# Kernel tuning notes

Measured on AMD Instinct MI355X. Metric: run time of the kernel, lower is better.

Reference implementation:

```python
import jax, jax.numpy as jnp
import numpy as np

EPS = 1e-12  # torch F.normalize eps

def _l2norm(t):
    # normalize over last axis (N), clamp norm like torch.nn.functional.normalize
    n = jnp.linalg.norm(t, axis=-1, keepdims=True)
    return t / jnp.maximum(n, EPS)

def setup_inputs() -> dict:
    key = jax.random.key(0)
    ks = jax.random.split(key, 4)
    B, N, D, H = 8, 4096, 768, 16
    x = jax.random.normal(ks[0], (B, N, D), dtype=jnp.float32)
    w_qkv = jax.random.normal(ks[1], (D, 3 * D), dtype=jnp.float32) * (D ** -0.5)
    temperature = jnp.ones((H, 1, 1), dtype=jnp.float32)
    w_proj = jax.random.normal(ks[2], (D, D), dtype=jnp.float32) * (D ** -0.5)
    b_proj = jnp.zeros((D,), dtype=jnp.float32)
    return {"x": x, "w_qkv": w_qkv, "temperature": temperature,
            "w_proj": w_proj, "b_proj": b_proj}

def reference(x, w_qkv, temperature, w_proj, b_proj):
    B, N, D = x.shape
    H = temperature.shape[0]
    C = D // H
    # qkv linear (no bias), split last dim as (3, H, C), move to (3, B, H, C, N)
    qkv = (x @ w_qkv).reshape(B, N, 3, H, C).transpose(2, 0, 3, 4, 1)
    q, k, v = qkv[0], qkv[1], qkv[2]            # each [B, H, C, N]
    q = _l2norm(q)
    k = _l2norm(k)
    # cross-covariance attention: small CxC matrix per head
    attn = jnp.einsum('bhcn,bhdn->bhcd', q, k) * temperature  # [B,H,C,C]
    attn = jax.nn.softmax(attn, axis=-1)
    out = jnp.einsum('bhcd,bhdn->bhcn', attn, v)  # [B,H,C,N]
    out = out.transpose(0, 3, 1, 2).reshape(B, N, D)  # B N (H C)
    return out @ w_proj + b_proj
```

## Files before the change

kernel.cpp:

```cpp
#include <hip/hip_runtime.h>
#include <stdint.h>

typedef __attribute__((ext_vector_type(4))) float          f32x4;
typedef __attribute__((ext_vector_type(8))) short          bf16x8;
typedef __attribute__((ext_vector_type(8))) unsigned short u16x8;
typedef __attribute__((ext_vector_type(4))) unsigned short u16x4;
typedef __attribute__((ext_vector_type(2))) long           longx2;

static __device__ __forceinline__ unsigned short f2bf(float f){
  uint32_t u = __builtin_bit_cast(uint32_t, f);
  u += 0x7FFFu + ((u >> 16) & 1u);
  return (unsigned short)(u >> 16);
}
static __device__ __forceinline__ float bf2f(unsigned short h){
  uint32_t u = ((uint32_t)h) << 16;
  return __builtin_bit_cast(float, u);
}

static __device__ __forceinline__ uint32_t f2e4m3(float x){
  uint32_t u = __builtin_bit_cast(uint32_t, x);
  uint32_t s = (u >> 24) & 0x80u;
  uint32_t a = u & 0x7FFFFFFFu;
  if (a >= 0x43E00000u) return s | 0x7Eu;
  int ebits = (int)(a >> 23);
  uint32_t mfull = (a & 0x7FFFFFu) | 0x800000u;
  int shift = (ebits >= 121) ? 20 : 20 + (121 - ebits);
  if (shift > 31) return s;
  uint32_t q = mfull >> shift;
  uint32_t rem = mfull & ((1u << shift) - 1u);
  uint32_t half = 1u << (shift - 1);
  q += (rem > half || (rem == half && (q & 1u)));
  if (ebits >= 121){
    uint32_t E = (uint32_t)(ebits - 121 + 1);
    if (q == 16u){ E += 1u; q = 8u; }
    uint32_t man = q - 8u;
    if (E > 15u || (E == 15u && man == 7u)) return s | 0x7Eu;
    return s | (E << 3) | man;
  } else {
    if (q >= 8u) return s | (1u << 3) | (q - 8u);
    return s | q;
  }
}
static __device__ __forceinline__ uint32_t pk4_e4m3(float a0, float a1, float a2, float a3){
#if __has_builtin(__builtin_amdgcn_cvt_pk_fp8_f32)
  uint32_t pk = (uint32_t)__builtin_amdgcn_cvt_pk_fp8_f32(a0, a1, 0, false);
  pk = (uint32_t)__builtin_amdgcn_cvt_pk_fp8_f32(a2, a3, (int)pk, true);
  return pk;
#else
  return f2e4m3(a0) | (f2e4m3(a1) << 8) | (f2e4m3(a2) << 16) | (f2e4m3(a3) << 24);
#endif
}

#define GLL(SRC, DST) __builtin_amdgcn_global_load_lds(                         \
    (const __attribute__((address_space(1))) unsigned int*)(SRC),               \
    (__attribute__((address_space(3))) unsigned int*)(DST), 16, 0, 0)

__global__ void k_pre(const float* __restrict__ x, const float* __restrict__ wqkv,
                      const float* __restrict__ wproj,
                      unsigned short* __restrict__ xbf, unsigned char* __restrict__ x8,
                      unsigned char* __restrict__ WT8, unsigned short* __restrict__ WpT,
                      unsigned short* __restrict__ WvB)
{
  __shared__ float tl[64][65];
  const int bx = blockIdx.x, t = threadIdx.x;
  if (bx < 12288){
    const long i = ((long)bx * 256 + t) * 8;
    const f32x4* p = (const f32x4*)(x + i);
    f32x4 a = p[0], b = p[1];
    u16x8 o;
    #pragma unroll
    for (int j = 0; j < 4; j++){ o[j] = f2bf(a[j]); o[4+j] = f2bf(b[j]); }
    *(u16x8*)(xbf + i) = o;
    uint32_t p0 = pk4_e4m3(a[0], a[1], a[2], a[3]);
    uint32_t p1 = pk4_e4m3(b[0], b[1], b[2], b[3]);
    *(uint32_t*)(x8 + i)     = p0;
    *(uint32_t*)(x8 + i + 4) = p1;
  } else if (bx < 12720){
    const int idx = bx - 12288;
    const int cb = idx % 36, rb = idx / 36;
    const int qk = (cb < 24);
    const float* in = qk ? wqkv : wproj;
    const int C = qk ? 2304 : 768;
    const int c0 = (qk ? cb : cb - 24) * 64, r0 = rb * 64;
    {
      const int lr = t >> 2, lc = (t & 3) * 16;
      const f32x4* s = (const f32x4*)(in + (long)(r0 + lr) * C + c0 + lc);
      #pragma unroll
      for (int q = 0; q < 4; q++){
        f32x4 v = s[q];
        #pragma unroll
        for (int j = 0; j < 4; j++) tl[lr][lc + q*4 + j] = v[j];
      }
    }
    __syncthreads();
    {
      const int oc = t >> 2, orr = (t & 3) * 16;
      if (qk){
        uint32_t w0 = pk4_e4m3(tl[orr+0][oc],  tl[orr+1][oc],  tl[orr+2][oc],  tl[orr+3][oc]);
        uint32_t w1 = pk4_e4m3(tl[orr+4][oc],  tl[orr+5][oc],  tl[orr+6][oc],  tl[orr+7][oc]);
        uint32_t w2 = pk4_e4m3(tl[orr+8][oc],  tl[orr+9][oc],  tl[orr+10][oc], tl[orr+11][oc]);
        uint32_t w3 = pk4_e4m3(tl[orr+12][oc], tl[orr+13][oc], tl[orr+14][oc], tl[orr+15][oc]);
        uint32_t* d = (uint32_t*)(WT8 + (long)(c0 + oc) * 768 + r0 + orr);
        d[0] = w0; d[1] = w1; d[2] = w2; d[3] = w3;
      } else {
        u16x8 o0, o1;
        #pragma unroll
        for (int i = 0; i < 8; i++){ o0[i] = f2bf(tl[orr + i][oc]); o1[i] = f2bf(tl[orr + 8 + i][oc]); }
        u16x8* dst = (u16x8*)(WpT + (long)(c0 + oc) * 768 + r0 + orr);
        dst[0] = o0; dst[1] = o1;
      }
    }
  } else {
    const long idx = ((long)(bx - 12720) * 256 + t) * 8;
    const int e = (int)(idx / 768), hd = (int)(idx - (long)e * 768);
    const float* s = wqkv + (long)e * 2304 + 1536 + hd;
    f32x4 a = *(const f32x4*)s, b = *(const f32x4*)(s + 4);
    u16x8 o;
    #pragma unroll
    for (int j = 0; j < 4; j++){ o[j] = f2bf(a[j]); o[4+j] = f2bf(b[j]); }
    *(u16x8*)(WvB + idx) = o;
  }
}

static __device__ __forceinline__ bf16x8 ldfrag(const char* slot, int row, int ko){
  const int k2 = (ko ^ (row >> 1)) & 3;
  return *(const bf16x8*)(slot + row*64 + k2*16);
}
static __device__ __forceinline__ longx2 ldfrag8(const char* slot, int row, int ko){
  const int k2 = (ko ^ (row >> 1)) & 3;
  return *(const longx2*)(slot + row*64 + k2*16);
}

static __device__ __forceinline__ void stg8(const unsigned char* __restrict__ G, int row0, int keB,
                                            char* lds_slot, int t){
  #pragma unroll
  for (int l = 0; l < 2; l++){
    const int r = l*128 + (t >> 2);
    const int c = (t & 3) ^ ((r >> 1) & 3);
    GLL((const char*)(G + (long)(row0 + r) * 768 + keB + c * 16),
        lds_slot + l*8192 + (t & 0x1C0) * 16);
  }
}

#define PH8(BUF, KK, MH, STAGE_STMT, WAIT_STMT) do {                           \
    longx2 af[4];                                                              \
    if (MH == 0) {                                                             \
      _Pragma("unroll")                                                        \
      for (int ni = 0; ni < 4; ni++)                                           \
        bq[ni] = ldfrag8(sB[BUF][KK], wn*64 + ni*16 + arow, ko);               \
    }                                                                          \
    _Pragma("unroll")                                                          \
    for (int mi = 0; mi < 4; mi++)                                             \
      af[mi] = ldfrag8(sA[BUF][KK], wm*128 + MH*64 + mi*16 + arow, ko);        \
    __builtin_amdgcn_s_barrier();                                              \
    __builtin_amdgcn_s_setprio(1);                                             \
    _Pragma("unroll")                                                          \
    for (int mi = 0; mi < 4; mi++)                                             \
      _Pragma("unroll")                                                        \
      for (int ni = 0; ni < 4; ni++){                                          \
        acc[MH*4+mi][ni] = __builtin_amdgcn_mfma_f32_16x16x32_fp8_fp8(         \
            af[mi][0], bq[ni][0], acc[MH*4+mi][ni], 0, 0, 0);                  \
        acc[MH*4+mi][ni] = __builtin_amdgcn_mfma_f32_16x16x32_fp8_fp8(         \
            af[mi][1], bq[ni][1], acc[MH*4+mi][ni], 0, 0, 0);                  \
      }                                                                        \
    __builtin_amdgcn_s_setprio(0);                                             \
    STAGE_STMT;                                                                \
    WAIT_STMT;                                                                 \
    __builtin_amdgcn_s_barrier();                                              \
  } while(0)

__global__ __launch_bounds__(512, 2)
void k_gemm256(const unsigned char* __restrict__ A8, const unsigned char* __restrict__ BT8,
               unsigned char* __restrict__ QT8, unsigned char* __restrict__ KT8,
               float* __restrict__ nrmp)
{
  __shared__ __attribute__((aligned(16))) char lds[131072];
  const int o  = blockIdx.x;
  const int wg = (o & 7) * 96 + (o >> 3);
  const int jt = wg % 6, mt = wg / 6;
  const int m0 = mt * 256, j0 = jt * 256;
  const int t = threadIdx.x, lane = t & 63, w = t >> 6;
  const int wm = w >> 2, wn = w & 3;
  const int arow = lane & 15, ko = lane >> 4;

  char* const sA[2][2] = {{lds,           lds + 16384},
                          {lds + 65536,   lds + 65536 + 16384}};
  char* const sB[2][2] = {{lds + 32768,   lds + 49152},
                          {lds + 65536 + 32768, lds + 65536 + 49152}};

  f32x4 acc[8][4] = {};

  stg8(BT8, j0, 0,   sB[0][0], t);
  stg8(A8,  m0, 0,   sA[0][0], t);
  stg8(BT8, j0, 64,  sB[0][1], t);
  stg8(A8,  m0, 64,  sA[0][1], t);
  stg8(BT8, j0, 128, sB[1][0], t);
  stg8(A8,  m0, 128, sA[1][0], t);
  stg8(BT8, j0, 192, sB[1][1], t);
  asm volatile("s_waitcnt vmcnt(6)" ::: "memory");
  __builtin_amdgcn_s_barrier();

  #pragma unroll 1
  for (int it = 0; it < 3; ++it){
    const int t1 = 2*it + 1, t2 = 2*it + 2, t3 = 2*it + 3;
    longx2 bq[4];
    PH8(0,0,0, { stg8(A8, m0, t1*128+64, sA[1][1], t); }, ;);
    PH8(0,0,1, { if (t2 < 6) stg8(BT8, j0, t2*128,    sB[0][0], t); }, ;);
    PH8(0,1,0, { if (t2 < 6) stg8(A8,  m0, t2*128,    sA[0][0], t); }, ;);
    PH8(0,1,1, { if (t2 < 6) stg8(BT8, j0, t2*128+64, sB[0][1], t); },
               { if (it == 2) asm volatile("s_waitcnt vmcnt(0)" ::: "memory");
                 else         asm volatile("s_waitcnt vmcnt(6)" ::: "memory"); });
    PH8(1,0,0, { if (t2 < 6) stg8(A8,  m0, t2*128+64, sA[0][1], t); }, ;);
    PH8(1,0,1, { if (t3 < 6) stg8(BT8, j0, t3*128,    sB[1][0], t); }, ;);
    PH8(1,1,0, { if (t3 < 6) stg8(A8,  m0, t3*128,    sA[1][0], t); }, ;);
    PH8(1,1,1, { if (t3 < 6) stg8(BT8, j0, t3*128+64, sB[1][1], t); },
               { if (it == 2) asm volatile("s_waitcnt vmcnt(0)" ::: "memory");
                 else         asm volatile("s_waitcnt vmcnt(6)" ::: "memory"); });
  }

  const int b = m0 >> 12;
  const int chunk = ((m0 & 4095) >> 7) + wm;
  #pragma unroll
  for (int ni = 0; ni < 4; ni++){
    float ss = 0.f;
    #pragma unroll
    for (int mi = 0; mi < 8; mi++)
      #pragma unroll
      for (int r = 0; r < 4; r++) ss += acc[mi][ni][r] * acc[mi][ni][r];
    ss += __shfl_xor(ss, 16);
    ss += __shfl_xor(ss, 32);
    if (lane < 16){
      const int jc = j0 + wn*64 + ni*16 + lane;
      const int s  = (jc >= 768);
      const int jl = jc - s * 768;
      const int h  = jl / 48;
      const int c  = jl - h * 48;
      nrmp[(long)(s*6144 + (b*16 + h)*48 + c)*32 + chunk] = ss;
    }
  }
  #pragma unroll
  for (int mi = 0; mi < 8; mi++){
    #pragma unroll
    for (int ni = 0; ni < 4; ni++){
      const int j  = wn*64 + ni*16 + (lane & 15);
      const int nl = wm*128 + mi*16 + (lane >> 4)*4;
      uint32_t pk = pk4_e4m3(acc[mi][ni][0], acc[mi][ni][1], acc[mi][ni][2], acc[mi][ni][3]);
      const int d = (nl >> 2) ^ ((j & 15) << 2);
      *(uint32_t*)(lds + (long)j*256 + (d << 2)) = pk;
    }
  }
  __syncthreads();
  for (int rr = 0; rr < 32; rr++){
    const int j  = w*32 + rr;
    const int jc = j0 + j;
    const int s  = (jc >= 768);
    const int jl = jc - s * 768;
    const int h  = jl / 48;
    const int c  = jl - h * 48;
    const int dp = lane ^ ((j & 15) << 2);
    uint32_t v = *(const uint32_t*)(lds + (long)j*256 + (dp << 2));
    *(uint32_t*)((s ? KT8 : QT8) + ((long)((b*16 + h)*48 + c) << 12) + (m0 & 4095) + lane*4) = v;
  }
}

static __device__ __forceinline__ void stageA512(const unsigned short* __restrict__ G, int row0, int ke,
                                                 char* slot, int t){
  const int r  = t >> 2;
  const int k2 = (t & 3) ^ ((r >> 1) & 3);
  GLL((const char*)(G + (long)(row0 + r) * 768 + ke + k2 * 8), slot + (t & 0x1C0) * 16);
}
static __device__ __forceinline__ void stageB512(const unsigned short* __restrict__ G, int row0, int ke,
                                                 char* slot, int t){
  #pragma unroll
  for (int l = 0; l < 2; l++){
    const int r  = l*128 + (t >> 2);
    const int k2 = (t & 3) ^ ((r >> 1) & 3);
    GLL((const char*)(G + (long)(row0 + r) * 768 + ke + k2 * 8), slot + l*8192 + (t & 0x1C0) * 16);
  }
}

#define VM0 asm volatile("s_waitcnt vmcnt(0)" ::: "memory")
#define VM3 asm volatile("s_waitcnt vmcnt(3)" ::: "memory")

#define PHASE1(CUR, STAGE_STMT, WAIT_STMT) do {                                \
    bf16x8 af[4], bq[4];                                                       \
    _Pragma("unroll")                                                          \
    for (int ni = 0; ni < 4; ni++)                                             \
      bq[ni] = ldfrag(sB[CUR], wn*64 + ni*16 + arow, ko);                      \
    _Pragma("unroll")                                                          \
    for (int mi = 0; mi < 4; mi++)                                             \
      af[mi] = ldfrag(sA[CUR], wm64 + mi*16 + arow, ko);                       \
    __builtin_amdgcn_s_barrier();                                              \
    __builtin_amdgcn_s_setprio(1);                                             \
    _Pragma("unroll")                                                          \
    for (int mi = 0; mi < 4; mi++)                                             \
      _Pragma("unroll")                                                        \
      for (int ni = 0; ni < 4; ni++)                                           \
        acc[mi][ni] = __builtin_amdgcn_mfma_f32_16x16x32_bf16(                 \
            af[mi], bq[ni], acc[mi][ni], 0, 0, 0);                             \
    __builtin_amdgcn_s_setprio(0);                                             \
    STAGE_STMT;                                                                \
    WAIT_STMT;                                                                 \
    __builtin_amdgcn_s_barrier();                                              \
  } while(0)

__global__ __launch_bounds__(512, 4)
void k_gemmP(const unsigned short* __restrict__ A, const unsigned short* __restrict__ BT,
             float* __restrict__ OUTF, const float* __restrict__ bias)
{
  __shared__ __attribute__((aligned(16))) char lds[73728];
  const int o  = blockIdx.x;
  const int wg = (o & 7) * 96 + (o >> 3);
  const int jt = wg % 3, mt = wg / 3;
  const int m0 = mt * 128, j0 = jt * 256;
  const int t = threadIdx.x, lane = t & 63, w = t >> 6;
  const int wm = w >> 2, wn = w & 3;
  const int wm64 = wm * 64;
  const int arow = lane & 15, ko = lane >> 4;
  const unsigned short* BTb = BT + ((long)(m0 >> 12)) * 589824;

  char* const sA[3] = {lds,          lds + 8192,          lds + 16384};
  char* const sB[3] = {lds + 24576,  lds + 24576 + 16384, lds + 24576 + 32768};

  f32x4 acc[4][4] = {};

  stageA512(A, m0, 0,  sA[0], t);  stageB512(BTb, j0, 0,  sB[0], t);
  stageA512(A, m0, 32, sA[1], t);  stageB512(BTb, j0, 32, sB[1], t);
  VM3;
  __builtin_amdgcn_s_barrier();

  #pragma unroll 1
  for (int g = 0; g < 7; ++g){
    const int kb = g * 96;
    PHASE1(0, { stageA512(A, m0, kb+64,  sA[2], t); stageB512(BTb, j0, kb+64,  sB[2], t); }, VM3);
    PHASE1(1, { stageA512(A, m0, kb+96,  sA[0], t); stageB512(BTb, j0, kb+96,  sB[0], t); }, VM3);
    PHASE1(2, { stageA512(A, m0, kb+128, sA[1], t); stageB512(BTb, j0, kb+128, sB[1], t); }, VM3);
  }
  PHASE1(0, { stageA512(A, m0, 736, sA[2], t); stageB512(BTb, j0, 736, sB[2], t); }, VM3);
  PHASE1(1, { ; }, VM0);
  PHASE1(2, { ; }, ;);

  #pragma unroll
  for (int mi = 0; mi < 4; mi++){
    #pragma unroll
    for (int ni = 0; ni < 4; ni++){
      const int jc = j0 + wn*64 + ni*16 + (lane & 15);
      const float bv = bias[jc];
      const long mr = (long)m0 + wm64 + mi*16 + (lane >> 4)*4;
      #pragma unroll
      for (int r = 0; r < 4; r++) OUTF[(mr + r) * 768 + jc] = acc[mi][ni][r] + bv;
    }
  }
}

__global__ __launch_bounds__(256)
void k_attn_part(const unsigned char* __restrict__ QT8, const unsigned char* __restrict__ KT8,
                 float* __restrict__ Spart)
{
  __shared__ float Sl[4][2304];
  const int bh = blockIdx.x, ksp = blockIdx.y;
  const int t = threadIdx.x, lane = t & 63, w = t >> 6;
  const unsigned char* qb = QT8 + ((long)bh * 48 << 12);
  const unsigned char* kb = KT8 + ((long)bh * 48 << 12);
  const int n00 = ksp * 1024 + w * 256;
  f32x4 acc[3][3] = {};
  for (int kt = 0; kt < 256; kt += 32){
    long af[3], bfr[3];
    #pragma unroll
    for (int ci = 0; ci < 3; ci++)
      af[ci]  = *(const long*)(qb + ((long)(ci*16 + (lane & 15)) << 12) + n00 + kt + (lane >> 4) * 8);
    #pragma unroll
    for (int di = 0; di < 3; di++)
      bfr[di] = *(const long*)(kb + ((long)(di*16 + (lane & 15)) << 12) + n00 + kt + (lane >> 4) * 8);
    #pragma unroll
    for (int ci = 0; ci < 3; ci++)
      #pragma unroll
      for (int di = 0; di < 3; di++)
        acc[ci][di] = __builtin_amdgcn_mfma_f32_16x16x32_fp8_fp8(af[ci], bfr[di], acc[ci][di], 0, 0, 0);
  }
  #pragma unroll
  for (int ci = 0; ci < 3; ci++)
    #pragma unroll
    for (int di = 0; di < 3; di++)
      #pragma unroll
      for (int r = 0; r < 4; r++)
        Sl[w][(ci*16 + (lane >> 4)*4 + r) * 48 + di*16 + (lane & 15)] = acc[ci][di][r];
  __syncthreads();
  float* outp = Spart + ((long)ksp * 128 + bh) * 2304;
  for (int idx = t; idx < 2304; idx += 256)
    outp[idx] = Sl[0][idx] + Sl[1][idx] + Sl[2][idx] + Sl[3][idx];
}

__global__ void k_softmax(const float* __restrict__ Spart, const float* __restrict__ nrmp,
                          const float* __restrict__ temp, unsigned short* __restrict__ attnT)
{
  __shared__ float invq[48], invk[48];
  const int bh = blockIdx.x, h = bh & 15;
  const int c = threadIdx.x;
  if (c < 48){
    float sq = 0.f, sk = 0.f;
    const float* pq = nrmp + (long)(bh*48 + c) * 32;
    const float* pk = nrmp + (long)(6144 + bh*48 + c) * 32;
    #pragma unroll
    for (int i = 0; i < 32; i++){ sq += pq[i]; sk += pk[i]; }
    invq[c] = 1.0f / fmaxf(sqrtf(sq), 1e-12f);
    invk[c] = 1.0f / fmaxf(sqrtf(sk), 1e-12f);
  }
  __syncthreads();
  if (c < 48){
    const float scq = invq[c] * temp[h];
    float row[48];
    #pragma unroll
    for (int d = 0; d < 48; d++){
      long base = ((long)bh * 48 + c) * 48 + d;
      float v = Spart[base] + Spart[base + 128L*2304] + Spart[base + 256L*2304] + Spart[base + 384L*2304];
      row[d] = v * scq * invk[d];
    }
    float mx = -1e30f;
    #pragma unroll
    for (int d = 0; d < 48; d++) mx = fmaxf(mx, row[d]);
    float s = 0.f;
    #pragma unroll
    for (int d = 0; d < 48; d++){ row[d] = expf(row[d] - mx); s += row[d]; }
    const float inv = 1.0f / s;
    unsigned short* ob = attnT + (long)bh * 48 * 64;
    #pragma unroll
    for (int d = 0; d < 48; d++) ob[d*64 + c] = f2bf(row[d] * inv);
    u16x8 z = {};
    *(u16x8*)(ob + c*64 + 48) = z;
    *(u16x8*)(ob + c*64 + 56) = z;
  }
}

__global__ __launch_bounds__(256)
void k_wmod2(const unsigned short* __restrict__ WpT, const unsigned short* __restrict__ attnT,
             unsigned short* __restrict__ WmodT)
{
  const int j0 = blockIdx.x * 256, h = blockIdx.y, b = blockIdx.z;
  const int t = threadIdx.x, lane = t & 63, w = t >> 6;
  const unsigned short* wp = WpT + h * 48;
  const unsigned short* ab = attnT + ((long)(b*16 + h)) * 48 * 64;
  f32x4 acc[4][3] = {};
  #pragma unroll
  for (int kt = 0; kt < 64; kt += 32){
    bf16x8 bfr[3];
    #pragma unroll
    for (int ni = 0; ni < 3; ni++)
      bfr[ni] = *(const bf16x8*)(ab + (ni*16 + (lane & 15))*64 + kt + (lane >> 4)*8);
    #pragma unroll
    for (int mi = 0; mi < 4; mi++){
      const int j = j0 + w*64 + mi*16 + (lane & 15);
      bf16x8 a = *(const bf16x8*)(wp + (long)j*768 + kt + (lane >> 4)*8);
      #pragma unroll
      for (int ni = 0; ni < 3; ni++)
        acc[mi][ni] = __builtin_amdgcn_mfma_f32_16x16x32_bf16(a, bfr[ni], acc[mi][ni], 0, 0, 0);
    }
  }
  #pragma unroll
  for (int mi = 0; mi < 4; mi++)
    #pragma unroll
    for (int ni = 0; ni < 3; ni++)
      #pragma unroll
      for (int r = 0; r < 4; r++){
        const int j = j0 + w*64 + mi*16 + (lane >> 4)*4 + r;
        const int d = ni*16 + (lane & 15);
        WmodT[(long)b*589824 + (long)j*768 + h*48 + d] = f2bf(acc[mi][ni][r]);
      }
}

__global__ __launch_bounds__(256)
void k_comb(const unsigned short* __restrict__ A, const unsigned short* __restrict__ BT,
            unsigned short* __restrict__ OUT)
{
  __shared__ unsigned short As[128 * 32];
  __shared__ unsigned short Bs[128 * 32];
  const int m0 = blockIdx.y * 128;
  const int j0 = blockIdx.x * 128;
  const int t = threadIdx.x;
  const int lane = t & 63;
  const int w = t >> 6, wm = w >> 1, wn = w & 1;

  f32x4 acc[4][4] = {};

  for (int kt = 0; kt < 768; kt += 32){
    if (kt) __syncthreads();
    #pragma unroll
    for (int i = 0; i < 2; i++){
      const char* ga = (const char*)A  + (long)(m0 + i*64 + (t >> 2)) * 1536 + kt*2 + (t & 3) * 16;
      const char* gb = (const char*)BT + (long)(j0 + i*64 + (t >> 2)) * 1536 + kt*2 + (t & 3) * 16;
      char* la = (char*)As + i*4096 + (t & 0xC0) * 16;
      char* lb = (char*)Bs + i*4096 + (t & 0xC0) * 16;
      GLL(ga, la);
      GLL(gb, lb);
    }
    __syncthreads();
    bf16x8 af[4], bfr[4];
    #pragma unroll
    for (int mi = 0; mi < 4; mi++)
      af[mi]  = *(const bf16x8*)&As[(wm*64 + mi*16 + (lane & 15)) * 32 + (lane >> 4) * 8];
    #pragma unroll
    for (int ni = 0; ni < 4; ni++)
      bfr[ni] = *(const bf16x8*)&Bs[(wn*64 + ni*16 + (lane & 15)) * 32 + (lane >> 4) * 8];
    #pragma unroll
    for (int mi = 0; mi < 4; mi++)
      #pragma unroll
      for (int ni = 0; ni < 4; ni++)
        acc[mi][ni] = __builtin_amdgcn_mfma_f32_16x16x32_bf16(af[mi], bfr[ni], acc[mi][ni], 0, 0, 0);
  }

  #pragma unroll
  for (int mi = 0; mi < 4; mi++)
    #pragma unroll
    for (int ni = 0; ni < 4; ni++){
      const int jc = j0 + wn*64 + ni*16 + (lane & 15);
      const long mr = (long)m0 + wm*64 + mi*16 + (lane >> 4) * 4;
      #pragma unroll
      for (int r = 0; r < 4; r++) OUT[(mr + r) * 768 + jc] = f2bf(acc[mi][ni][r]);
    }
}

extern "C" void kernel_launch(void* const* d_in, const int* in_sizes, int n_in,
                              void* d_out, int out_size, void* d_ws, size_t ws_size,
                              hipStream_t stream)
{
  (void)in_sizes; (void)n_in; (void)out_size; (void)ws_size;
  const float* x      = (const float*)d_in[0];
  const float* w_qkv  = (const float*)d_in[1];
  const float* temp   = (const float*)d_in[2];
  const float* w_proj = (const float*)d_in[3];
  const float* b_proj = (const float*)d_in[4];
  float* outF = (float*)d_out;

  char* ws = (char*)d_ws;
  size_t off = 0;
  auto alloc = [&](size_t bytes)->char*{ char* p = ws + off; off += (bytes + 255) & ~(size_t)255; return p; };

  unsigned short* x_bf  = (unsigned short*)alloc(50331648);
  unsigned char*  x8    = (unsigned char*)alloc(25165824);
  unsigned char*  WT8   = (unsigned char*)alloc(1179648);
  unsigned short* WpT   = (unsigned short*)alloc(1179648);
  unsigned short* WvB   = (unsigned short*)alloc(1179648);
  unsigned char*  QT8   = (unsigned char*)alloc(50331648);
  unsigned char*  KT8   = QT8 + (long)6144 * 4096;
  float* nrmp           = (float*)alloc(12288L * 32 * 4);
  float* Spart          = (float*)alloc(4L * 128 * 2304 * 4);
  unsigned short* attnT = (unsigned short*)alloc(786432);
  unsigned short* WmodT = (unsigned short*)alloc(9437184);
  unsigned short* WcombT= (unsigned short*)alloc(9437184);

  k_pre<<<13008, 256, 0, stream>>>(x, w_qkv, w_proj, x_bf, x8, WT8, WpT, WvB);
  k_gemm256<<<768, 512, 0, stream>>>(x8, WT8, QT8, KT8, nrmp);
  k_attn_part<<<dim3(128, 4), 256, 0, stream>>>(QT8, KT8, Spart);
  k_softmax<<<128, 64, 0, stream>>>(Spart, nrmp, temp, attnT);
  k_wmod2<<<dim3(3, 16, 8), 256, 0, stream>>>(WpT, attnT, WmodT);
  k_comb<<<dim3(6, 48), 256, 0, stream>>>(WmodT, WvB, WcombT);
  k_gemmP<<<768, 512, 0, stream>>>(x_bf, WcombT, outF, b_proj);
}
```

Before: 211.0 us.

## Fuse softmax and Wmod into attn partial via last-block counter; pipeline k_comb

The softmax and the per-head Wmod GEMM kernels are folded into k_attn_part. The last of the four split-N blocks for each (b,h), found with an atomic counter, reduces the partial scores, applies softmax into LDS and computes that head's slice of WmodT. Separately, k_comb switches to a triple-buffered LDS pipeline with swizzled staging and the PHASE1 macro, replacing its single-buffer sync loop. This removes two kernel launches and the attnT round trip, but it adds a memset, atomics and a serialized tail in only 128 blocks.

```diff
diff --git a/kernel.cpp b/kernel.cpp
--- a/kernel.cpp
+++ b/kernel.cpp
@@ -11,10 +11,6 @@
   uint32_t u = __builtin_bit_cast(uint32_t, f);
   u += 0x7FFFu + ((u >> 16) & 1u);
   return (unsigned short)(u >> 16);
-}
-static __device__ __forceinline__ float bf2f(unsigned short h){
-  uint32_t u = ((uint32_t)h) << 16;
-  return __builtin_bit_cast(float, u);
 }
 
 static __device__ __forceinline__ uint32_t f2e4m3(float x){
@@ -71,10 +67,8 @@
     #pragma unroll
     for (int j = 0; j < 4; j++){ o[j] = f2bf(a[j]); o[4+j] = f2bf(b[j]); }
     *(u16x8*)(xbf + i) = o;
-    uint32_t p0 = pk4_e4m3(a[0], a[1], a[2], a[3]);
-    uint32_t p1 = pk4_e4m3(b[0], b[1], b[2], b[3]);
-    *(uint32_t*)(x8 + i)     = p0;
-    *(uint32_t*)(x8 + i + 4) = p1;
+    *(uint32_t*)(x8 + i)     = pk4_e4m3(a[0], a[1], a[2], a[3]);
+    *(uint32_t*)(x8 + i + 4) = pk4_e4m3(b[0], b[1], b[2], b[3]);
   } else if (bx < 12720){
     const int idx = bx - 12288;
     const int cb = idx % 36, rb = idx / 36;
@@ -278,9 +272,20 @@
     GLL((const char*)(G + (long)(row0 + r) * 768 + ke + k2 * 8), slot + l*8192 + (t & 0x1C0) * 16);
   }
 }
+static __device__ __forceinline__ void stg128c(const unsigned short* __restrict__ G, int row0, int ke,
+                                               char* slot, int t){
+  #pragma unroll
+  for (int l = 0; l < 2; l++){
+    const int r  = ((l*4 + (t >> 6)) << 4) + ((t & 63) >> 2);
+    const int k2 = (t & 3) ^ ((r >> 1) & 3);
+    GLL((const char*)(G + (long)(row0 + r) * 768 + ke + k2 * 8),
+        slot + l*4096 + (t & 0x3C0) * 16);
+  }
+}
 
 #define VM0 asm volatile("s_waitcnt vmcnt(0)" ::: "memory")
 #define VM3 asm volatile("s_waitcnt vmcnt(3)" ::: "memory")
+#define VM4 asm volatile("s_waitcnt vmcnt(4)" ::: "memory")
 
 #define PHASE1(CUR, STAGE_STMT, WAIT_STMT) do {                                \
     bf16x8 af[4], bq[4];                                                       \
@@ -355,9 +360,13 @@
 
 __global__ __launch_bounds__(256)
 void k_attn_part(const unsigned char* __restrict__ QT8, const unsigned char* __restrict__ KT8,
-                 float* __restrict__ Spart)
+                 float* __restrict__ Spart, const float* __restrict__ nrmp,
+                 const unsigned short* __restrict__ WpT, const float* __restrict__ temp,
+                 unsigned short* __restrict__ WmodT, int* __restrict__ cnt)
 {
   __shared__ float Sl[4][2304];
+  __shared__ float invq_s[48], invk_s[48];
+  __shared__ int lastf;
   const int bh = blockIdx.x, ksp = blockIdx.y;
   const int t = threadIdx.x, lane = t & 63, w = t >> 6;
   const unsigned char* qb = QT8 + ((long)bh * 48 << 12);
@@ -389,32 +398,36 @@
   float* outp = Spart + ((long)ksp * 128 + bh) * 2304;
   for (int idx = t; idx < 2304; idx += 256)
     outp[idx] = Sl[0][idx] + Sl[1][idx] + Sl[2][idx] + Sl[3][idx];
-}
-
-__global__ void k_softmax(const float* __restrict__ Spart, const float* __restrict__ nrmp,
-                          const float* __restrict__ temp, unsigned short* __restrict__ attnT)
-{
-  __shared__ float invq[48], invk[48];
-  const int bh = blockIdx.x, h = bh & 15;
-  const int c = threadIdx.x;
-  if (c < 48){
+
+  if (t == 0){
+    __threadfence();
+    lastf = (atomicAdd(&cnt[bh], 1) == 3);
+  }
+  __syncthreads();
+  if (!lastf) return;
+  __threadfence();
+
+  const int h = bh & 15;
+  unsigned short* aT = (unsigned short*)&Sl[0][0];
+  if (t < 48){
     float sq = 0.f, sk = 0.f;
-    const float* pq = nrmp + (long)(bh*48 + c) * 32;
-    const float* pk = nrmp + (long)(6144 + bh*48 + c) * 32;
+    const float* pq = nrmp + (long)(bh*48 + t) * 32;
+    const float* pk = nrmp + (long)(6144 + bh*48 + t) * 32;
     #pragma unroll
     for (int i = 0; i < 32; i++){ sq += pq[i]; sk += pk[i]; }
-    invq[c] = 1.0f / fmaxf(sqrtf(sq), 1e-12f);
-    invk[c] = 1.0f / fmaxf(sqrtf(sk), 1e-12f);
+    invq_s[t] = 1.0f / fmaxf(sqrtf(sq), 1e-12f);
+    invk_s[t] = 1.0f / fmaxf(sqrtf(sk), 1e-12f);
   }
   __syncthreads();
-  if (c < 48){
-    const float scq = invq[c] * temp[h];
+  if (t < 48){
+    const int c = t;
+    const float scq = invq_s[c] * temp[h];
     float row[48];
     #pragma unroll
     for (int d = 0; d < 48; d++){
       long base = ((long)bh * 48 + c) * 48 + d;
       float v = Spart[base] + Spart[base + 128L*2304] + Spart[base + 256L*2304] + Spart[base + 384L*2304];
-      row[d] = v * scq * invk[d];
+      row[d] = v * scq * invk_s[d];
     }
     float mx = -1e30f;
     #pragma unroll
@@ -423,97 +436,85 @@
     #pragma unroll
     for (int d = 0; d < 48; d++){ row[d] = expf(row[d] - mx); s += row[d]; }
     const float inv = 1.0f / s;
-    unsigned short* ob = attnT + (long)bh * 48 * 64;
-    #pragma unroll
-    for (int d = 0; d < 48; d++) ob[d*64 + c] = f2bf(row[d] * inv);
+    #pragma unroll
+    for (int d = 0; d < 48; d++) aT[d*64 + c] = f2bf(row[d] * inv);
     u16x8 z = {};
-    *(u16x8*)(ob + c*64 + 48) = z;
-    *(u16x8*)(ob + c*64 + 56) = z;
-  }
-}
-
-__global__ __launch_bounds__(256)
-void k_wmod2(const unsigned short* __restrict__ WpT, const unsigned short* __restrict__ attnT,
-             unsigned short* __restrict__ WmodT)
-{
-  const int j0 = blockIdx.x * 256, h = blockIdx.y, b = blockIdx.z;
-  const int t = threadIdx.x, lane = t & 63, w = t >> 6;
+    *(u16x8*)(aT + c*64 + 48) = z;
+    *(u16x8*)(aT + c*64 + 56) = z;
+  }
+  __syncthreads();
   const unsigned short* wp = WpT + h * 48;
-  const unsigned short* ab = attnT + ((long)(b*16 + h)) * 48 * 64;
-  f32x4 acc[4][3] = {};
-  #pragma unroll
-  for (int kt = 0; kt < 64; kt += 32){
-    bf16x8 bfr[3];
-    #pragma unroll
-    for (int ni = 0; ni < 3; ni++)
-      bfr[ni] = *(const bf16x8*)(ab + (ni*16 + (lane & 15))*64 + kt + (lane >> 4)*8);
-    #pragma unroll
-    for (int mi = 0; mi < 4; mi++){
-      const int j = j0 + w*64 + mi*16 + (lane & 15);
-      bf16x8 a = *(const bf16x8*)(wp + (long)j*768 + kt + (lane >> 4)*8);
+  unsigned short* wmb = WmodT + (long)(bh >> 4) * 589824;
+  #pragma unroll 1
+  for (int ch = 0; ch < 3; ch++){
+    f32x4 a2[4][3] = {};
+    #pragma unroll
+    for (int kt = 0; kt < 64; kt += 32){
+      bf16x8 bfr2[3];
       #pragma unroll
       for (int ni = 0; ni < 3; ni++)
-        acc[mi][ni] = __builtin_amdgcn_mfma_f32_16x16x32_bf16(a, bfr[ni], acc[mi][ni], 0, 0, 0);
-    }
-  }
-  #pragma unroll
-  for (int mi = 0; mi < 4; mi++)
-    #pragma unroll
-    for (int ni = 0; ni < 3; ni++)
-      #pragma unroll
-      for (int r = 0; r < 4; r++){
-        const int j = j0 + w*64 + mi*16 + (lane >> 4)*4 + r;
-        const int d = ni*16 + (lane & 15);
-        WmodT[(long)b*589824 + (long)j*768 + h*48 + d] = f2bf(acc[mi][ni][r]);
+        bfr2[ni] = *(const bf16x8*)(aT + (ni*16 + (lane & 15))*64 + kt + (lane >> 4)*8);
+      #pragma unroll
+      for (int mi = 0; mi < 4; mi++){
+        const int j = w*192 + ch*64 + mi*16 + (lane & 15);
+        bf16x8 a = *(const bf16x8*)(wp + (long)j*768 + kt + (lane >> 4)*8);
+        #pragma unroll
+        for (int ni = 0; ni < 3; ni++)
+          a2[mi][ni] = __builtin_amdgcn_mfma_f32_16x16x32_bf16(a, bfr2[ni], a2[mi][ni], 0, 0, 0);
       }
-}
-
-__global__ __launch_bounds__(256)
+    }
+    #pragma unroll
+    for (int mi = 0; mi < 4; mi++)
+      #pragma unroll
+      for (int ni = 0; ni < 3; ni++)
+        #pragma unroll
+        for (int r = 0; r < 4; r++){
+          const int j = w*192 + ch*64 + mi*16 + (lane >> 4)*4 + r;
+          const int d = ni*16 + (lane & 15);
+          wmb[(long)j*768 + h*48 + d] = f2bf(a2[mi][ni][r]);
+        }
+  }
+}
+
+__global__ __launch_bounds__(256, 3)
 void k_comb(const unsigned short* __restrict__ A, const unsigned short* __restrict__ BT,
             unsigned short* __restrict__ OUT)
 {
-  __shared__ unsigned short As[128 * 32];
-  __shared__ unsigned short Bs[128 * 32];
+  __shared__ __attribute__((aligned(16))) char lds[49152];
   const int m0 = blockIdx.y * 128;
   const int j0 = blockIdx.x * 128;
-  const int t = threadIdx.x;
-  const int lane = t & 63;
-  const int w = t >> 6, wm = w >> 1, wn = w & 1;
+  const int t = threadIdx.x, lane = t & 63, w = t >> 6;
+  const int wm = w >> 1, wn = w & 1;
+  const int wm64 = wm * 64;
+  const int arow = lane & 15, ko = lane >> 4;
+
+  char* const sA[3] = {lds,          lds + 8192,   lds + 16384};
+  char* const sB[3] = {lds + 24576,  lds + 32768,  lds + 40960};
 
   f32x4 acc[4][4] = {};
 
-  for (int kt = 0; kt < 768; kt += 32){
-    if (kt) __syncthreads();
-    #pragma unroll
-    for (int i = 0; i < 2; i++){
-      const char* ga = (const char*)A  + (long)(m0 + i*64 + (t >> 2)) * 1536 + kt*2 + (t & 3) * 16;
-      const char* gb = (const char*)BT + (long)(j0 + i*64 + (t >> 2)) * 1536 + kt*2 + (t & 3) * 16;
-      char* la = (char*)As + i*4096 + (t & 0xC0) * 16;
-      char* lb = (char*)Bs + i*4096 + (t & 0xC0) * 16;
-      GLL(ga, la);
-      GLL(gb, lb);
-    }
-    __syncthreads();
-    bf16x8 af[4], bfr[4];
-    #pragma unroll
-    for (int mi = 0; mi < 4; mi++)
-      af[mi]  = *(const bf16x8*)&As[(wm*64 + mi*16 + (lane & 15)) * 32 + (lane >> 4) * 8];
-    #pragma unroll
-    for (int ni = 0; ni < 4; ni++)
-      bfr[ni] = *(const bf16x8*)&Bs[(wn*64 + ni*16 + (lane & 15)) * 32 + (lane >> 4) * 8];
-    #pragma unroll
-    for (int mi = 0; mi < 4; mi++)
-      #pragma unroll
-      for (int ni = 0; ni < 4; ni++)
-        acc[mi][ni] = __builtin_amdgcn_mfma_f32_16x16x32_bf16(af[mi], bfr[ni], acc[mi][ni], 0, 0, 0);
-  }
+  stg128c(A, m0, 0,  sA[0], t);  stg128c(BT, j0, 0,  sB[0], t);
+  stg128c(A, m0, 32, sA[1], t);  stg128c(BT, j0, 32, sB[1], t);
+  VM4;
+  __builtin_amdgcn_s_barrier();
+
+  #pragma unroll 1
+  for (int g = 0; g < 7; ++g){
+    const int kb = g * 96;
+    PHASE1(0, { stg128c(A, m0, kb+64,  sA[2], t); stg128c(BT, j0, kb+64,  sB[2], t); }, VM4);
+    PHASE1(1, { stg128c(A, m0, kb+96,  sA[0], t); stg128c(BT, j0, kb+96,  sB[0], t); }, VM4);
+    PHASE1(2, { stg128c(A, m0, kb+128, sA[1], t); stg128c(BT, j0, kb+128, sB[1], t); }, VM4);
+  }
+  PHASE1(0, { stg128c(A, m0, 736, sA[2], t); stg128c(BT, j0, 736, sB[2], t); }, VM4);
+  PHASE1(1, { ; }, VM0);
+  PHASE1(2, { ; }, ;);
 
   #pragma unroll
   for (int mi = 0; mi < 4; mi++)
     #pragma unroll
     for (int ni = 0; ni < 4; ni++){
       const int jc = j0 + wn*64 + ni*16 + (lane & 15);
-      const long mr = (long)m0 + wm*64 + mi*16 + (lane >> 4) * 4;
+      const long mr = (long)m0 + wm64 + mi*16 + (lane >> 4) * 4;
       #pragma unroll
       for (int r = 0; r < 4; r++) OUT[(mr + r) * 768 + jc] = f2bf(acc[mi][ni][r]);
     }
@@ -544,15 +545,14 @@
   unsigned char*  KT8   = QT8 + (long)6144 * 4096;
   float* nrmp           = (float*)alloc(12288L * 32 * 4);
   float* Spart          = (float*)alloc(4L * 128 * 2304 * 4);
-  unsigned short* attnT = (unsigned short*)alloc(786432);
   unsigned short* WmodT = (unsigned short*)alloc(9437184);
   unsigned short* WcombT= (unsigned short*)alloc(9437184);
-
+  int* cnt              = (int*)alloc(512);
+
+  hipMemsetAsync(cnt, 0, 512, stream);
   k_pre<<<13008, 256, 0, stream>>>(x, w_qkv, w_proj, x_bf, x8, WT8, WpT, WvB);
   k_gemm256<<<768, 512, 0, stream>>>(x8, WT8, QT8, KT8, nrmp);
-  k_attn_part<<<dim3(128, 4), 256, 0, stream>>>(QT8, KT8, Spart);
-  k_softmax<<<128, 64, 0, stream>>>(Spart, nrmp, temp, attnT);
-  k_wmod2<<<dim3(3, 16, 8), 256, 0, stream>>>(WpT, attnT, WmodT);
+  k_attn_part<<<dim3(128, 4), 256, 0, stream>>>(QT8, KT8, Spart, nrmp, WpT, temp, WmodT, cnt);
   k_comb<<<dim3(6, 48), 256, 0, stream>>>(WmodT, WvB, WcombT);
   k_gemmP<<<768, 512, 0, stream>>>(x_bf, WcombT, outF, b_proj);
 }
```

After: 232.8 us. +10.3%, slower.

## Triple-buffer k_comb GEMM with async global-to-LDS prefetch and swizzled layout

Applied to the files above, without the earlier changes.

Rewrites the k_comb bf16 GEMM main loop to use a three-stage LDS ring buffer. The loads for stages k+2 are issued while stage k is computed, reusing the PHASE1 macro with vmcnt waits and a single s_barrier per step instead of two __syncthreads. It also applies an XOR-swizzled LDS layout to cut bank conflicts and sets launch_bounds occupancy to 3 blocks. This raises LDS use to 48KB per block, which may limit occupancy, and relies on the vmcnt counts matching the number of outstanding loads.

```diff
diff --git a/kernel.cpp b/kernel.cpp
--- a/kernel.cpp
+++ b/kernel.cpp
@@ -11,10 +11,6 @@
   uint32_t u = __builtin_bit_cast(uint32_t, f);
   u += 0x7FFFu + ((u >> 16) & 1u);
   return (unsigned short)(u >> 16);
-}
-static __device__ __forceinline__ float bf2f(unsigned short h){
-  uint32_t u = ((uint32_t)h) << 16;
-  return __builtin_bit_cast(float, u);
 }
 
 static __device__ __forceinline__ uint32_t f2e4m3(float x){
@@ -71,10 +67,8 @@
     #pragma unroll
     for (int j = 0; j < 4; j++){ o[j] = f2bf(a[j]); o[4+j] = f2bf(b[j]); }
     *(u16x8*)(xbf + i) = o;
-    uint32_t p0 = pk4_e4m3(a[0], a[1], a[2], a[3]);
-    uint32_t p1 = pk4_e4m3(b[0], b[1], b[2], b[3]);
-    *(uint32_t*)(x8 + i)     = p0;
-    *(uint32_t*)(x8 + i + 4) = p1;
+    *(uint32_t*)(x8 + i)     = pk4_e4m3(a[0], a[1], a[2], a[3]);
+    *(uint32_t*)(x8 + i + 4) = pk4_e4m3(b[0], b[1], b[2], b[3]);
   } else if (bx < 12720){
     const int idx = bx - 12288;
     const int cb = idx % 36, rb = idx / 36;
@@ -278,9 +272,20 @@
     GLL((const char*)(G + (long)(row0 + r) * 768 + ke + k2 * 8), slot + l*8192 + (t & 0x1C0) * 16);
   }
 }
+static __device__ __forceinline__ void stg128c(const unsigned short* __restrict__ G, int row0, int ke,
+                                               char* slot, int t){
+  #pragma unroll
+  for (int l = 0; l < 2; l++){
+    const int r  = ((l*4 + (t >> 6)) << 4) + ((t & 63) >> 2);
+    const int k2 = (t & 3) ^ ((r >> 1) & 3);
+    GLL((const char*)(G + (long)(row0 + r) * 768 + ke + k2 * 8),
+        slot + l*4096 + (t & 0x3C0) * 16);
+  }
+}
 
 #define VM0 asm volatile("s_waitcnt vmcnt(0)" ::: "memory")
 #define VM3 asm volatile("s_waitcnt vmcnt(3)" ::: "memory")
+#define VM4 asm volatile("s_waitcnt vmcnt(4)" ::: "memory")
 
 #define PHASE1(CUR, STAGE_STMT, WAIT_STMT) do {                                \
     bf16x8 af[4], bq[4];                                                       \
@@ -468,52 +473,45 @@
       }
 }
 
-__global__ __launch_bounds__(256)
+__global__ __launch_bounds__(256, 3)
 void k_comb(const unsigned short* __restrict__ A, const unsigned short* __restrict__ BT,
             unsigned short* __restrict__ OUT)
 {
-  __shared__ unsigned short As[128 * 32];
-  __shared__ unsigned short Bs[128 * 32];
+  __shared__ __attribute__((aligned(16))) char lds[49152];
   const int m0 = blockIdx.y * 128;
   const int j0 = blockIdx.x * 128;
-  const int t = threadIdx.x;
-  const int lane = t & 63;
-  const int w = t >> 6, wm = w >> 1, wn = w & 1;
+  const int t = threadIdx.x, lane = t & 63, w = t >> 6;
+  const int wm = w >> 1, wn = w & 1;
+  const int wm64 = wm * 64;
+  const int arow = lane & 15, ko = lane >> 4;
+
+  char* const sA[3] = {lds,          lds + 8192,   lds + 16384};
+  char* const sB[3] = {lds + 24576,  lds + 32768,  lds + 40960};
 
   f32x4 acc[4][4] = {};
 
-  for (int kt = 0; kt < 768; kt += 32){
-    if (kt) __syncthreads();
-    #pragma unroll
-    for (int i = 0; i < 2; i++){
-      const char* ga = (const char*)A  + (long)(m0 + i*64 + (t >> 2)) * 1536 + kt*2 + (t & 3) * 16;
-      const char* gb = (const char*)BT + (long)(j0 + i*64 + (t >> 2)) * 1536 + kt*2 + (t & 3) * 16;
-      char* la = (char*)As + i*4096 + (t & 0xC0) * 16;
-      char* lb = (char*)Bs + i*4096 + (t & 0xC0) * 16;
-      GLL(ga, la);
-      GLL(gb, lb);
-    }
-    __syncthreads();
-    bf16x8 af[4], bfr[4];
-    #pragma unroll
-    for (int mi = 0; mi < 4; mi++)
-      af[mi]  = *(const bf16x8*)&As[(wm*64 + mi*16 + (lane & 15)) * 32 + (lane >> 4) * 8];
-    #pragma unroll
-    for (int ni = 0; ni < 4; ni++)
-      bfr[ni] = *(const bf16x8*)&Bs[(wn*64 + ni*16 + (lane & 15)) * 32 + (lane >> 4) * 8];
-    #pragma unroll
-    for (int mi = 0; mi < 4; mi++)
-      #pragma unroll
-      for (int ni = 0; ni < 4; ni++)
-        acc[mi][ni] = __builtin_amdgcn_mfma_f32_16x16x32_bf16(af[mi], bfr[ni], acc[mi][ni], 0, 0, 0);
-  }
+  stg128c(A, m0, 0,  sA[0], t);  stg128c(BT, j0, 0,  sB[0], t);
+  stg128c(A, m0, 32, sA[1], t);  stg128c(BT, j0, 32, sB[1], t);
+  VM4;
+  __builtin_amdgcn_s_barrier();
+
+  #pragma unroll 1
+  for (int g = 0; g < 7; ++g){
+    const int kb = g * 96;
+    PHASE1(0, { stg128c(A, m0, kb+64,  sA[2], t); stg128c(BT, j0, kb+64,  sB[2], t); }, VM4);
+    PHASE1(1, { stg128c(A, m0, kb+96,  sA[0], t); stg128c(BT, j0, kb+96,  sB[0], t); }, VM4);
+    PHASE1(2, { stg128c(A, m0, kb+128, sA[1], t); stg128c(BT, j0, kb+128, sB[1], t); }, VM4);
+  }
+  PHASE1(0, { stg128c(A, m0, 736, sA[2], t); stg128c(BT, j0, 736, sB[2], t); }, VM4);
+  PHASE1(1, { ; }, VM0);
+  PHASE1(2, { ; }, ;);
 
   #pragma unroll
   for (int mi = 0; mi < 4; mi++)
     #pragma unroll
     for (int ni = 0; ni < 4; ni++){
       const int jc = j0 + wn*64 + ni*16 + (lane & 15);
-      const long mr = (long)m0 + wm*64 + mi*16 + (lane >> 4) * 4;
+      const long mr = (long)m0 + wm64 + mi*16 + (lane >> 4) * 4;
       #pragma unroll
       for (int r = 0; r < 4; r++) OUT[(mr + r) * 768 + jc] = f2bf(acc[mi][ni][r]);
     }
```

Result: no change. 208.8 us (-1.0%).
